# Performance work log

Hardware: AMD Instinct MI355X
Metric: run time of the kernel (lower is better)

Reference implementation:

```python
import jax, jax.numpy as jnp
import numpy as np

N_NODES = 50000
N_EDGES = 800000
F_IN = 128
HEADS = 4
C = 64  # hidden_dim // heads
HIDDEN = HEADS * C
NUM_GRAPHS = 256
NEG_SLOPE = 0.2


def setup_inputs() -> dict:
    key = jax.random.key(0)
    ks = jax.random.split(key, 10)
    x = jax.random.normal(ks[0], (N_NODES, F_IN), dtype=jnp.float32)
    edge_index = jax.random.randint(ks[1], (2, N_EDGES), 0, N_NODES, dtype=jnp.int64)
    edge_attr = jax.random.normal(ks[2], (N_EDGES, 8), dtype=jnp.float32)
    batch = jnp.sort(jax.random.randint(ks[3], (N_NODES,), 0, NUM_GRAPHS, dtype=jnp.int64))
    # GATConv params (PyG: lin weight, att_src/att_dst, bias) + fc head
    W = jax.random.normal(ks[4], (F_IN, HIDDEN), dtype=jnp.float32) / np.sqrt(F_IN)
    att_src = jax.random.normal(ks[5], (HEADS, C), dtype=jnp.float32) / np.sqrt(C)
    att_dst = jax.random.normal(ks[6], (HEADS, C), dtype=jnp.float32) / np.sqrt(C)
    bias = jax.random.normal(ks[7], (HIDDEN,), dtype=jnp.float32) * 0.01
    fc_w = jax.random.normal(ks[8], (1, HIDDEN), dtype=jnp.float32) / np.sqrt(HIDDEN)
    fc_b = jax.random.normal(ks[9], (1,), dtype=jnp.float32) * 0.01
    return {"x": x, "edge_index": edge_index, "edge_attr": edge_attr, "batch": batch,
            "W": W, "att_src": att_src, "att_dst": att_dst, "bias": bias,
            "fc_w": fc_w, "fc_b": fc_b}


def reference(x, edge_index, edge_attr, batch, W, att_src, att_dst, bias, fc_w, fc_b):
    N = x.shape[0]
    # add self loops
    loops = jnp.arange(N, dtype=edge_index.dtype)
    src = jnp.concatenate([edge_index[0], loops])  # [E+N]
    dst = jnp.concatenate([edge_index[1], loops])
    # GATConv: linear transform per head
    h = (x @ W).reshape(N, HEADS, C)  # [N,H,C]
    a_src = jnp.einsum('nhc,hc->nh', h, att_src)  # [N,H]
    a_dst = jnp.einsum('nhc,hc->nh', h, att_dst)
    e = a_src[src] + a_dst[dst]  # [E,H]
    e = jnp.where(e > 0, e, NEG_SLOPE * e)  # leaky_relu
    # segment softmax over destination neighborhoods (self loops guarantee nonempty)
    m = jax.ops.segment_max(e, dst, num_segments=N)
    ee = jnp.exp(e - m[dst])
    s = jax.ops.segment_sum(ee, dst, num_segments=N)
    alpha = ee / s[dst]  # [E,H]
    msg = h[src] * alpha[:, :, None]  # [E,H,C]
    out = jax.ops.segment_sum(msg, dst, num_segments=N).reshape(N, HIDDEN) + bias
    out = jax.nn.elu(out)
    # global mean pool
    sums = jax.ops.segment_sum(out, batch, num_segments=NUM_GRAPHS)
    counts = jax.ops.segment_sum(jnp.ones((N,), out.dtype), batch, num_segments=NUM_GRAPHS)
    pooled = sums / jnp.maximum(counts, 1.0)[:, None]  # [G,HIDDEN]
    o = pooled @ fc_w.T + fc_b  # [G,1]
    return o.reshape(-1)
```

## Files before the change

kernel.cpp:

```cpp
#include <hip/hip_runtime.h>
#include <hip/hip_bf16.h>
#include <math.h>

#define HEADS   4
#define HIDDEN  256
#define FIN     128
#define NGRAPH  256
#define WPB     4
#define HISTB   512
#define PCHUNK  64

using frag_ab = __attribute__((ext_vector_type(8))) short;
using frag_cd = __attribute__((ext_vector_type(4))) float;

__device__ __forceinline__ float bf2f(unsigned short u) {
  union { unsigned int i; float f; } v; v.i = ((unsigned int)u) << 16; return v.f;
}
__device__ __forceinline__ unsigned short f2bf(float f) {
  union { float f; unsigned int i; } v; v.f = f;
  unsigned int b = v.i;
  b += 0x7FFFu + ((b >> 16) & 1u);
  return (unsigned short)(b >> 16);
}

__global__ __launch_bounds__(256) void k_prep(const float* __restrict__ W,
                                              unsigned short* __restrict__ Bf)
{
  int id = blockIdx.x * 256 + threadIdx.x;
  if (id >= 16 * 4 * 64) return;
  int l = id & 63, ks = (id >> 6) & 3, nfg = id >> 8;
  int col = nfg * 16 + (l & 15);
  int k0  = ks * 32 + (l >> 4) * 8;
  unsigned short v[8];
  #pragma unroll
  for (int j = 0; j < 8; ++j) v[j] = f2bf(W[(k0 + j) * HIDDEN + col]);
  *(uint4*)(Bf + (size_t)id * 8) = *(const uint4*)v;
}

__global__ __launch_bounds__(256) void k_gemmhist(
    const float* __restrict__ x, const unsigned short* __restrict__ Bf,
    const float* __restrict__ att_s, const float* __restrict__ att_d,
    unsigned short* __restrict__ h16, float* __restrict__ a_src, float* __restrict__ a_dst,
    const int* __restrict__ ei, int* __restrict__ count,
    int nNodes, int E, int gemmBlocks)
{
  __shared__ unsigned short As[32 * FIN];
  const int t = threadIdx.x;

  if (blockIdx.x >= gemmBlocks) {
    int i = (blockIdx.x - gemmBlocks) * 256 + t;
    int stride = HISTB * 256;
    for (int e = i; e < E; e += stride) atomicAdd(&count[ei[E + e]], 1);
    return;
  }

  const int n0 = blockIdx.x * 32;

  {
    const int row = t >> 3;
    const int g   = n0 + row;
    const int c0  = (t & 7) * 16;
    float4 f0, f1, f2, f3;
    if (g < nNodes) {
      const float* xr = x + (size_t)g * FIN + c0;
      f0 = *(const float4*)(xr + 0);  f1 = *(const float4*)(xr + 4);
      f2 = *(const float4*)(xr + 8);  f3 = *(const float4*)(xr + 12);
    } else {
      f0 = f1 = f2 = f3 = make_float4(0.f, 0.f, 0.f, 0.f);
    }
    unsigned short u[16];
    u[0]=f2bf(f0.x); u[1]=f2bf(f0.y); u[2]=f2bf(f0.z); u[3]=f2bf(f0.w);
    u[4]=f2bf(f1.x); u[5]=f2bf(f1.y); u[6]=f2bf(f1.z); u[7]=f2bf(f1.w);
    u[8]=f2bf(f2.x); u[9]=f2bf(f2.y); u[10]=f2bf(f2.z); u[11]=f2bf(f2.w);
    u[12]=f2bf(f3.x); u[13]=f2bf(f3.y); u[14]=f2bf(f3.z); u[15]=f2bf(f3.w);
    const int sw = (row & 7) << 4;
    char* base = (char*)As + row * 256;
    *(uint4*)(base + (((t & 7) * 32)      ^ sw)) = *(const uint4*)(u + 0);
    *(uint4*)(base + (((t & 7) * 32 + 16) ^ sw)) = *(const uint4*)(u + 8);
  }
  __syncthreads();

  const int w    = t >> 6;
  const int l    = t & 63;
  const int lrow = l & 15;

  frag_ab bfr[4][4];
  #pragma unroll
  for (int nf = 0; nf < 4; ++nf)
    #pragma unroll
    for (int ks = 0; ks < 4; ++ks)
      bfr[nf][ks] = *(const frag_ab*)(Bf + (size_t)(((w * 4 + nf) * 4 + ks) * 64 + l) * 8);

  frag_ab afr[2][4];
  const int lsw = (lrow & 7) << 4;
  #pragma unroll
  for (int mf = 0; mf < 2; ++mf)
    #pragma unroll
    for (int ks = 0; ks < 4; ++ks) {
      int byte = (mf * 16 + lrow) * 256 + ((ks * 64 + (l >> 4) * 16) ^ lsw);
      afr[mf][ks] = *(const frag_ab*)((const char*)As + byte);
    }

  frag_cd acc[2][4];
  #pragma unroll
  for (int mf = 0; mf < 2; ++mf)
    #pragma unroll
    for (int nf = 0; nf < 4; ++nf)
      acc[mf][nf] = (frag_cd){0.f, 0.f, 0.f, 0.f};
  #pragma unroll
  for (int ks = 0; ks < 4; ++ks)
    #pragma unroll
    for (int mf = 0; mf < 2; ++mf)
      #pragma unroll
      for (int nf = 0; nf < 4; ++nf)
        acc[mf][nf] = __builtin_amdgcn_mfma_f32_16x16x32_bf16(
            afr[mf][ks], bfr[nf][ks], acc[mf][nf], 0, 0, 0);

  float asw[4], adw[4];
  #pragma unroll
  for (int nf = 0; nf < 4; ++nf) {
    asw[nf] = att_s[w * 64 + nf * 16 + lrow];
    adw[nf] = att_d[w * 64 + nf * 16 + lrow];
  }

  #pragma unroll
  for (int mf = 0; mf < 2; ++mf) {
    #pragma unroll
    for (int r = 0; r < 4; ++r) {
      const int rowg = n0 + mf * 16 + (l >> 4) * 4 + r;
      if (rowg < nNodes) {
        #pragma unroll
        for (int nf = 0; nf < 4; ++nf)
          h16[(size_t)rowg * HIDDEN + w * 64 + nf * 16 + lrow] = f2bf(acc[mf][nf][r]);
      }
      float ss = 0.f, sd = 0.f;
      #pragma unroll
      for (int nf = 0; nf < 4; ++nf) {
        ss = fmaf(acc[mf][nf][r], asw[nf], ss);
        sd = fmaf(acc[mf][nf][r], adw[nf], sd);
      }
      #pragma unroll
      for (int off2 = 1; off2 <= 8; off2 <<= 1) {
        ss += __shfl_xor(ss, off2, 64);
        sd += __shfl_xor(sd, off2, 64);
      }
      if (lrow == 0 && rowg < nNodes) {
        a_src[rowg * HEADS + w] = ss;
        a_dst[rowg * HEADS + w] = sd;
      }
    }
  }
}

__global__ __launch_bounds__(256) void k_scan1(const int* __restrict__ cnt,
                                               int* __restrict__ offs,
                                               int* __restrict__ bsum, int n)
{
  int t = threadIdx.x, b = blockIdx.x;
  int i = b * 256 + t;
  int v = (i < n) ? cnt[i] + 1 : 0;
  int sc = v;
  #pragma unroll
  for (int d2 = 1; d2 < 64; d2 <<= 1) {
    int u = __shfl_up(sc, d2, 64);
    if ((t & 63) >= d2) sc += u;
  }
  __shared__ int wsum[4];
  if ((t & 63) == 63) wsum[t >> 6] = sc;
  __syncthreads();
  int base = 0;
  for (int w = 0; w < (t >> 6); ++w) base += wsum[w];
  int incl = sc + base;
  if (i < n) offs[i] = incl - v;
  if (t == 255) bsum[b] = incl;
}

__global__ __launch_bounds__(256) void k_scan23(int* __restrict__ offs,
                                                const int* __restrict__ bsum,
                                                int* __restrict__ cursor,
                                                int n, int nb, int total)
{
  int t = threadIdx.x, b = blockIdx.x;
  float dummy; (void)dummy;
  int partial = 0;
  for (int j = t; j < b; j += 256) partial += bsum[j];
  #pragma unroll
  for (int off2 = 32; off2; off2 >>= 1) partial += __shfl_xor(partial, off2, 64);
  __shared__ int ws4[4];
  if ((t & 63) == 0) ws4[t >> 6] = partial;
  __syncthreads();
  int blockBase = ws4[0] + ws4[1] + ws4[2] + ws4[3];

  int i = b * 256 + t;
  if (i < n) {
    int o = offs[i] + blockBase;
    offs[i] = o;
    cursor[i] = o;
  }
  if (i == 0) offs[n] = total;
}

__global__ __launch_bounds__(256) void k_scatter(
    const int* __restrict__ ei, int* __restrict__ cursor,
    int* __restrict__ ssrc, int E, int N)
{
  int e = blockIdx.x * 256 + threadIdx.x;
  int tot = E + N;
  if (e >= tot) return;
  int s, d;
  if (e < E) { s = ei[e]; d = ei[E + e]; }
  else       { s = e - E; d = s; }
  int pos = atomicAdd(&cursor[d], 1);
  ssrc[pos] = s;
}

__global__ __launch_bounds__(256) void k_agg(
    const unsigned short* __restrict__ h16, const int* __restrict__ offs,
    const int* __restrict__ ssrc,
    const float* __restrict__ a_src, const float* __restrict__ a_dst,
    const float* __restrict__ bias,
    unsigned short* __restrict__ outn, int N)
{
  const int wid0 = blockIdx.x * WPB + (threadIdx.x >> 6);
  if (wid0 >= N) return;
  const int wid  = __builtin_amdgcn_readfirstlane(wid0);
  const int lane = threadIdx.x & 63;
  const int head = lane >> 4;
  const int col  = lane << 2;

  const int beg = offs[wid], end = offs[wid + 1];
  const float ad = a_dst[wid * 4 + head];

  float4 acc = make_float4(0.f, 0.f, 0.f, 0.f);
  float den = 0.f;
  int k = beg;

  for (; k + 8 <= end; k += 8) {
    int s0 = ssrc[k + 0], s1 = ssrc[k + 1], s2 = ssrc[k + 2], s3 = ssrc[k + 3];
    int s4 = ssrc[k + 4], s5 = ssrc[k + 5], s6 = ssrc[k + 6], s7 = ssrc[k + 7];
    float e0 = a_src[s0 * 4 + head], e1 = a_src[s1 * 4 + head];
    float e2 = a_src[s2 * 4 + head], e3 = a_src[s3 * 4 + head];
    float e4 = a_src[s4 * 4 + head], e5 = a_src[s5 * 4 + head];
    float e6 = a_src[s6 * 4 + head], e7 = a_src[s7 * 4 + head];
    ushort4 h0 = *(const ushort4*)(h16 + (size_t)s0 * HIDDEN + col);
    ushort4 h1 = *(const ushort4*)(h16 + (size_t)s1 * HIDDEN + col);
    ushort4 h2 = *(const ushort4*)(h16 + (size_t)s2 * HIDDEN + col);
    ushort4 h3 = *(const ushort4*)(h16 + (size_t)s3 * HIDDEN + col);
    ushort4 h4 = *(const ushort4*)(h16 + (size_t)s4 * HIDDEN + col);
    ushort4 h5 = *(const ushort4*)(h16 + (size_t)s5 * HIDDEN + col);
    ushort4 h6 = *(const ushort4*)(h16 + (size_t)s6 * HIDDEN + col);
    ushort4 h7 = *(const ushort4*)(h16 + (size_t)s7 * HIDDEN + col);
    float w0, w1, w2, w3, w4, w5, w6, w7;
    e0 += ad; e0 = e0 > 0.f ? e0 : 0.2f * e0; w0 = __expf(e0);
    e1 += ad; e1 = e1 > 0.f ? e1 : 0.2f * e1; w1 = __expf(e1);
    e2 += ad; e2 = e2 > 0.f ? e2 : 0.2f * e2; w2 = __expf(e2);
    e3 += ad; e3 = e3 > 0.f ? e3 : 0.2f * e3; w3 = __expf(e3);
    e4 += ad; e4 = e4 > 0.f ? e4 : 0.2f * e4; w4 = __expf(e4);
    e5 += ad; e5 = e5 > 0.f ? e5 : 0.2f * e5; w5 = __expf(e5);
    e6 += ad; e6 = e6 > 0.f ? e6 : 0.2f * e6; w6 = __expf(e6);
    e7 += ad; e7 = e7 > 0.f ? e7 : 0.2f * e7; w7 = __expf(e7);
    den += ((w0 + w1) + (w2 + w3)) + ((w4 + w5) + (w6 + w7));
    acc.x = fmaf(bf2f(h0.x), w0, acc.x); acc.y = fmaf(bf2f(h0.y), w0, acc.y);
    acc.z = fmaf(bf2f(h0.z), w0, acc.z); acc.w = fmaf(bf2f(h0.w), w0, acc.w);
    acc.x = fmaf(bf2f(h1.x), w1, acc.x); acc.y = fmaf(bf2f(h1.y), w1, acc.y);
    acc.z = fmaf(bf2f(h1.z), w1, acc.z); acc.w = fmaf(bf2f(h1.w), w1, acc.w);
    acc.x = fmaf(bf2f(h2.x), w2, acc.x); acc.y = fmaf(bf2f(h2.y), w2, acc.y);
    acc.z = fmaf(bf2f(h2.z), w2, acc.z); acc.w = fmaf(bf2f(h2.w), w2, acc.w);
    acc.x = fmaf(bf2f(h3.x), w3, acc.x); acc.y = fmaf(bf2f(h3.y), w3, acc.y);
    acc.z = fmaf(bf2f(h3.z), w3, acc.z); acc.w = fmaf(bf2f(h3.w), w3, acc.w);
    acc.x = fmaf(bf2f(h4.x), w4, acc.x); acc.y = fmaf(bf2f(h4.y), w4, acc.y);
    acc.z = fmaf(bf2f(h4.z), w4, acc.z); acc.w = fmaf(bf2f(h4.w), w4, acc.w);
    acc.x = fmaf(bf2f(h5.x), w5, acc.x); acc.y = fmaf(bf2f(h5.y), w5, acc.y);
    acc.z = fmaf(bf2f(h5.z), w5, acc.z); acc.w = fmaf(bf2f(h5.w), w5, acc.w);
    acc.x = fmaf(bf2f(h6.x), w6, acc.x); acc.y = fmaf(bf2f(h6.y), w6, acc.y);
    acc.z = fmaf(bf2f(h6.z), w6, acc.z); acc.w = fmaf(bf2f(h6.w), w6, acc.w);
    acc.x = fmaf(bf2f(h7.x), w7, acc.x); acc.y = fmaf(bf2f(h7.y), w7, acc.y);
    acc.z = fmaf(bf2f(h7.z), w7, acc.z); acc.w = fmaf(bf2f(h7.w), w7, acc.w);
  }
  for (; k < end; ++k) {
    int s = ssrc[k];
    float e = a_src[s * 4 + head] + ad;
    e = e > 0.f ? e : 0.2f * e;
    float w = __expf(e);
    ushort4 hv = *(const ushort4*)(h16 + (size_t)s * HIDDEN + col);
    den += w;
    acc.x = fmaf(bf2f(hv.x), w, acc.x); acc.y = fmaf(bf2f(hv.y), w, acc.y);
    acc.z = fmaf(bf2f(hv.z), w, acc.z); acc.w = fmaf(bf2f(hv.w), w, acc.w);
  }

  const float inv = 1.f / den;
  float4 bv = *(const float4*)&bias[col];
  float4 o;
  o.x = fmaf(acc.x, inv, bv.x); o.x = o.x > 0.f ? o.x : expm1f(o.x);
  o.y = fmaf(acc.y, inv, bv.y); o.y = o.y > 0.f ? o.y : expm1f(o.y);
  o.z = fmaf(acc.z, inv, bv.z); o.z = o.z > 0.f ? o.z : expm1f(o.z);
  o.w = fmaf(acc.w, inv, bv.w); o.w = o.w > 0.f ? o.w : expm1f(o.w);

  ushort4 ov;
  ov.x = f2bf(o.x); ov.y = f2bf(o.y); ov.z = f2bf(o.z); ov.w = f2bf(o.w);
  *(ushort4*)(outn + (size_t)wid * HIDDEN + col) = ov;
}

__global__ __launch_bounds__(256) void k_poolp(
    const unsigned short* __restrict__ outn, const int* __restrict__ batch,
    float* __restrict__ pooled, float* __restrict__ cntg, int N)
{
  const int t = threadIdx.x;
  const int n0 = blockIdx.x * PCHUNK;
  if (n0 >= N) return;
  const int n1 = (n0 + PCHUNK < N) ? n0 + PCHUNK : N;

  int cur = batch[n0];
  float run = 0.f;
  int runlen = 0;
  int n = n0;
  for (; n + 4 <= n1; n += 4) {
    unsigned short r0 = outn[(size_t)(n + 0) * HIDDEN + t];
    unsigned short r1 = outn[(size_t)(n + 1) * HIDDEN + t];
    unsigned short r2 = outn[(size_t)(n + 2) * HIDDEN + t];
    unsigned short r3 = outn[(size_t)(n + 3) * HIDDEN + t];
    int g0 = batch[n + 0], g3 = batch[n + 3];
    if (g0 == cur && g3 == cur) {
      run += (bf2f(r0) + bf2f(r1)) + (bf2f(r2) + bf2f(r3));
      runlen += 4;
    } else {
      unsigned short rr[4] = {r0, r1, r2, r3};
      #pragma unroll
      for (int j = 0; j < 4; ++j) {
        int g = batch[n + j];
        if (g != cur) {
          atomicAdd(&pooled[cur * HIDDEN + t], run);
          if (t == 0) atomicAdd(&cntg[cur], (float)runlen);
          run = 0.f; runlen = 0; cur = g;
        }
        run += bf2f(rr[j]); runlen++;
      }
    }
  }
  for (; n < n1; ++n) {
    int g = batch[n];
    if (g != cur) {
      atomicAdd(&pooled[cur * HIDDEN + t], run);
      if (t == 0) atomicAdd(&cntg[cur], (float)runlen);
      run = 0.f; runlen = 0; cur = g;
    }
    run += bf2f(outn[(size_t)n * HIDDEN + t]); runlen++;
  }
  atomicAdd(&pooled[cur * HIDDEN + t], run);
  if (t == 0) atomicAdd(&cntg[cur], (float)runlen);
}

__global__ __launch_bounds__(64) void k_fc(
    const float* __restrict__ pooled, const float* __restrict__ cntg,
    const float* __restrict__ fc_w, const float* __restrict__ fc_b, float* __restrict__ out)
{
  int g = blockIdx.x, l = threadIdx.x;
  float acc = 0.f;
  #pragma unroll
  for (int j = 0; j < HIDDEN / 64; ++j) acc += pooled[g * HIDDEN + j * 64 + l] * fc_w[j * 64 + l];
  #pragma unroll
  for (int off2 = 32; off2; off2 >>= 1) acc += __shfl_xor(acc, off2, 64);
  if (l == 0) out[g] = acc / fmaxf(cntg[g], 1.0f) + fc_b[0];
}

extern "C" void kernel_launch(void* const* d_in, const int* in_sizes, int n_in,
                              void* d_out, int out_size, void* d_ws, size_t ws_size,
                              hipStream_t stream)
{
  const float* x     = (const float*)d_in[0];
  const int*   ei    = (const int*)  d_in[1];
  const int*   batch = (const int*)  d_in[3];
  const float* W     = (const float*)d_in[4];
  const float* att_s = (const float*)d_in[5];
  const float* att_d = (const float*)d_in[6];
  const float* bias  = (const float*)d_in[7];
  const float* fc_w  = (const float*)d_in[8];
  const float* fc_b  = (const float*)d_in[9];
  float* out = (float*)d_out;

  const int N   = in_sizes[0] / FIN;
  const int E   = in_sizes[1] / 2;
  const int TOT = E + N;

  char* p = (char*)d_ws;
  size_t o = 0;
  auto alloc = [&](size_t bytes) -> void* {
    void* r = p + o;
    o = (o + bytes + 255) & ~(size_t)255;
    return r;
  };
  int*   count  = (int*)  alloc((size_t)N * sizeof(int));
  float* pooled = (float*)alloc((size_t)NGRAPH * HIDDEN * sizeof(float));
  float* cntg   = (float*)alloc((size_t)NGRAPH * sizeof(float));
  size_t zeroBytes = o;
  unsigned short* h16 = (unsigned short*)alloc((size_t)N * HIDDEN * sizeof(unsigned short));
  unsigned short* Bf  = (unsigned short*)alloc((size_t)FIN * HIDDEN * sizeof(unsigned short));
  float* a_src  = (float*)alloc((size_t)N * 4 * sizeof(float));
  float* a_dst  = (float*)alloc((size_t)N * 4 * sizeof(float));
  int*   offs   = (int*)  alloc((size_t)(N + 1) * sizeof(int));
  int*   cursor = (int*)  alloc((size_t)N * sizeof(int));
  int*   bsum   = (int*)  alloc(4096);
  int*   ssrc   = (int*)  alloc((size_t)TOT * sizeof(int));
  unsigned short* outn = (unsigned short*)alloc((size_t)N * HIDDEN * sizeof(unsigned short));
  (void)n_in; (void)out_size; (void)ws_size;

  (void)hipMemsetAsync(d_ws, 0, zeroBytes, stream);

  const int gemmBlocks = (N + 31) / 32;
  hipLaunchKernelGGL(k_prep, dim3(16), dim3(256), 0, stream, W, Bf);
  hipLaunchKernelGGL(k_gemmhist, dim3(gemmBlocks + HISTB), dim3(256), 0, stream,
                     x, Bf, att_s, att_d, h16, a_src, a_dst, ei, count, N, E, gemmBlocks);
  const int sb = (N + 255) / 256;
  hipLaunchKernelGGL(k_scan1, dim3(sb), dim3(256), 0, stream, count, offs, bsum, N);
  hipLaunchKernelGGL(k_scan23, dim3(sb), dim3(256), 0, stream, offs, bsum, cursor, N, sb, TOT);
  hipLaunchKernelGGL(k_scatter, dim3((TOT + 255) / 256), dim3(256), 0, stream,
                     ei, cursor, ssrc, E, N);
  hipLaunchKernelGGL(k_agg, dim3((N + WPB - 1) / WPB), dim3(256), 0, stream,
                     h16, offs, ssrc, a_src, a_dst, bias, outn, N);
  hipLaunchKernelGGL(k_poolp, dim3((N + PCHUNK - 1) / PCHUNK), dim3(256), 0, stream,
                     outn, batch, pooled, cntg, N);
  hipLaunchKernelGGL(k_fc, dim3(NGRAPH), dim3(64), 0, stream,
                     pooled, cntg, fc_w, fc_b, out);
}
```

Baseline: 276.9 us.

## Precompute edge attention weights in scatter, merge scans, deepen agg gather unroll

Computes the per-edge exp(leaky_relu(a_src+a_dst)) for all four heads in the scatter kernel and stores it as a float4 per CSR slot, so the aggregation kernel reads weights contiguously instead of gathering a_src and recomputing exp per lane. Merges the two scan kernels into one, where each block sums all preceding counts directly, removing a launch at the cost of O(N) redundant reads per block. The aggregation loop is unrolled to 16 with a 4-wide tail to expose more outstanding gathers. It adds a 16-byte-per-edge write and read of the weight array, plus more register pressure from the wider unroll.

```diff
diff --git a/kernel.cpp b/kernel.cpp
--- a/kernel.cpp
+++ b/kernel.cpp
@@ -152,13 +152,23 @@
   }
 }
 
-__global__ __launch_bounds__(256) void k_scan1(const int* __restrict__ cnt,
-                                               int* __restrict__ offs,
-                                               int* __restrict__ bsum, int n)
-{
-  int t = threadIdx.x, b = blockIdx.x;
-  int i = b * 256 + t;
-  int v = (i < n) ? cnt[i] + 1 : 0;
+__global__ __launch_bounds__(256) void k_scan(const int* __restrict__ cnt,
+                                              int* __restrict__ offs,
+                                              int* __restrict__ cursor,
+                                              int n, int total)
+{
+  const int t = threadIdx.x, b = blockIdx.x;
+  int partial = 0;
+  for (int j = t; j < b * 256; j += 256) partial += cnt[j];
+  #pragma unroll
+  for (int off2 = 32; off2; off2 >>= 1) partial += __shfl_xor(partial, off2, 64);
+  __shared__ int bs4[4];
+  if ((t & 63) == 0) bs4[t >> 6] = partial;
+  __syncthreads();
+  const int base = bs4[0] + bs4[1] + bs4[2] + bs4[3] + b * 256;
+
+  const int i = b * 256 + t;
+  const int v = (i < n) ? cnt[i] + 1 : 0;
   int sc = v;
   #pragma unroll
   for (int d2 = 1; d2 < 64; d2 <<= 1) {
@@ -168,41 +178,18 @@
   __shared__ int wsum[4];
   if ((t & 63) == 63) wsum[t >> 6] = sc;
   __syncthreads();
-  int base = 0;
-  for (int w = 0; w < (t >> 6); ++w) base += wsum[w];
-  int incl = sc + base;
-  if (i < n) offs[i] = incl - v;
-  if (t == 255) bsum[b] = incl;
-}
-
-__global__ __launch_bounds__(256) void k_scan23(int* __restrict__ offs,
-                                                const int* __restrict__ bsum,
-                                                int* __restrict__ cursor,
-                                                int n, int nb, int total)
-{
-  int t = threadIdx.x, b = blockIdx.x;
-  float dummy; (void)dummy;
-  int partial = 0;
-  for (int j = t; j < b; j += 256) partial += bsum[j];
-  #pragma unroll
-  for (int off2 = 32; off2; off2 >>= 1) partial += __shfl_xor(partial, off2, 64);
-  __shared__ int ws4[4];
-  if ((t & 63) == 0) ws4[t >> 6] = partial;
-  __syncthreads();
-  int blockBase = ws4[0] + ws4[1] + ws4[2] + ws4[3];
-
-  int i = b * 256 + t;
-  if (i < n) {
-    int o = offs[i] + blockBase;
-    offs[i] = o;
-    cursor[i] = o;
-  }
+  int wb = 0;
+  for (int w = 0; w < (t >> 6); ++w) wb += wsum[w];
+  const int excl = base + wb + sc - v;
+  if (i < n) { offs[i] = excl; cursor[i] = excl; }
   if (i == 0) offs[n] = total;
 }
 
 __global__ __launch_bounds__(256) void k_scatter(
-    const int* __restrict__ ei, int* __restrict__ cursor,
-    int* __restrict__ ssrc, int E, int N)
+    const int* __restrict__ ei,
+    const float4* __restrict__ a_src4, const float4* __restrict__ a_dst4,
+    int* __restrict__ cursor,
+    int* __restrict__ ssrc, float4* __restrict__ see, int E, int N)
 {
   int e = blockIdx.x * 256 + threadIdx.x;
   int tot = E + N;
@@ -210,14 +197,21 @@
   int s, d;
   if (e < E) { s = ei[e]; d = ei[E + e]; }
   else       { s = e - E; d = s; }
+  float4 as = a_src4[s];
+  float4 ad = a_dst4[d];
+  float4 w; float v;
+  v = as.x + ad.x; v = v > 0.f ? v : 0.2f * v; w.x = __expf(v);
+  v = as.y + ad.y; v = v > 0.f ? v : 0.2f * v; w.y = __expf(v);
+  v = as.z + ad.z; v = v > 0.f ? v : 0.2f * v; w.z = __expf(v);
+  v = as.w + ad.w; v = v > 0.f ? v : 0.2f * v; w.w = __expf(v);
   int pos = atomicAdd(&cursor[d], 1);
   ssrc[pos] = s;
+  see[pos] = w;
 }
 
 __global__ __launch_bounds__(256) void k_agg(
     const unsigned short* __restrict__ h16, const int* __restrict__ offs,
-    const int* __restrict__ ssrc,
-    const float* __restrict__ a_src, const float* __restrict__ a_dst,
+    const int* __restrict__ ssrc, const float* __restrict__ see,
     const float* __restrict__ bias,
     unsigned short* __restrict__ outn, int N)
 {
@@ -229,59 +223,54 @@
   const int col  = lane << 2;
 
   const int beg = offs[wid], end = offs[wid + 1];
-  const float ad = a_dst[wid * 4 + head];
 
   float4 acc = make_float4(0.f, 0.f, 0.f, 0.f);
   float den = 0.f;
   int k = beg;
 
-  for (; k + 8 <= end; k += 8) {
-    int s0 = ssrc[k + 0], s1 = ssrc[k + 1], s2 = ssrc[k + 2], s3 = ssrc[k + 3];
-    int s4 = ssrc[k + 4], s5 = ssrc[k + 5], s6 = ssrc[k + 6], s7 = ssrc[k + 7];
-    float e0 = a_src[s0 * 4 + head], e1 = a_src[s1 * 4 + head];
-    float e2 = a_src[s2 * 4 + head], e3 = a_src[s3 * 4 + head];
-    float e4 = a_src[s4 * 4 + head], e5 = a_src[s5 * 4 + head];
-    float e6 = a_src[s6 * 4 + head], e7 = a_src[s7 * 4 + head];
-    ushort4 h0 = *(const ushort4*)(h16 + (size_t)s0 * HIDDEN + col);
-    ushort4 h1 = *(const ushort4*)(h16 + (size_t)s1 * HIDDEN + col);
-    ushort4 h2 = *(const ushort4*)(h16 + (size_t)s2 * HIDDEN + col);
-    ushort4 h3 = *(const ushort4*)(h16 + (size_t)s3 * HIDDEN + col);
-    ushort4 h4 = *(const ushort4*)(h16 + (size_t)s4 * HIDDEN + col);
-    ushort4 h5 = *(const ushort4*)(h16 + (size_t)s5 * HIDDEN + col);
-    ushort4 h6 = *(const ushort4*)(h16 + (size_t)s6 * HIDDEN + col);
-    ushort4 h7 = *(const ushort4*)(h16 + (size_t)s7 * HIDDEN + col);
-    float w0, w1, w2, w3, w4, w5, w6, w7;
-    e0 += ad; e0 = e0 > 0.f ? e0 : 0.2f * e0; w0 = __expf(e0);
-    e1 += ad; e1 = e1 > 0.f ? e1 : 0.2f * e1; w1 = __expf(e1);
-    e2 += ad; e2 = e2 > 0.f ? e2 : 0.2f * e2; w2 = __expf(e2);
-    e3 += ad; e3 = e3 > 0.f ? e3 : 0.2f * e3; w3 = __expf(e3);
-    e4 += ad; e4 = e4 > 0.f ? e4 : 0.2f * e4; w4 = __expf(e4);
-    e5 += ad; e5 = e5 > 0.f ? e5 : 0.2f * e5; w5 = __expf(e5);
-    e6 += ad; e6 = e6 > 0.f ? e6 : 0.2f * e6; w6 = __expf(e6);
-    e7 += ad; e7 = e7 > 0.f ? e7 : 0.2f * e7; w7 = __expf(e7);
-    den += ((w0 + w1) + (w2 + w3)) + ((w4 + w5) + (w6 + w7));
-    acc.x = fmaf(bf2f(h0.x), w0, acc.x); acc.y = fmaf(bf2f(h0.y), w0, acc.y);
-    acc.z = fmaf(bf2f(h0.z), w0, acc.z); acc.w = fmaf(bf2f(h0.w), w0, acc.w);
-    acc.x = fmaf(bf2f(h1.x), w1, acc.x); acc.y = fmaf(bf2f(h1.y), w1, acc.y);
-    acc.z = fmaf(bf2f(h1.z), w1, acc.z); acc.w = fmaf(bf2f(h1.w), w1, acc.w);
-    acc.x = fmaf(bf2f(h2.x), w2, acc.x); acc.y = fmaf(bf2f(h2.y), w2, acc.y);
-    acc.z = fmaf(bf2f(h2.z), w2, acc.z); acc.w = fmaf(bf2f(h2.w), w2, acc.w);
-    acc.x = fmaf(bf2f(h3.x), w3, acc.x); acc.y = fmaf(bf2f(h3.y), w3, acc.y);
-    acc.z = fmaf(bf2f(h3.z), w3, acc.z); acc.w = fmaf(bf2f(h3.w), w3, acc.w);
-    acc.x = fmaf(bf2f(h4.x), w4, acc.x); acc.y = fmaf(bf2f(h4.y), w4, acc.y);
-    acc.z = fmaf(bf2f(h4.z), w4, acc.z); acc.w = fmaf(bf2f(h4.w), w4, acc.w);
-    acc.x = fmaf(bf2f(h5.x), w5, acc.x); acc.y = fmaf(bf2f(h5.y), w5, acc.y);
-    acc.z = fmaf(bf2f(h5.z), w5, acc.z); acc.w = fmaf(bf2f(h5.w), w5, acc.w);
-    acc.x = fmaf(bf2f(h6.x), w6, acc.x); acc.y = fmaf(bf2f(h6.y), w6, acc.y);
-    acc.z = fmaf(bf2f(h6.z), w6, acc.z); acc.w = fmaf(bf2f(h6.w), w6, acc.w);
-    acc.x = fmaf(bf2f(h7.x), w7, acc.x); acc.y = fmaf(bf2f(h7.y), w7, acc.y);
-    acc.z = fmaf(bf2f(h7.z), w7, acc.z); acc.w = fmaf(bf2f(h7.w), w7, acc.w);
+  for (; k + 16 <= end; k += 16) {
+    int s[16];
+    #pragma unroll
+    for (int j = 0; j < 16; ++j) s[j] = ssrc[k + j];
+    float w[16];
+    #pragma unroll
+    for (int j = 0; j < 16; ++j) w[j] = see[(size_t)(k + j) * 4 + head];
+    ushort4 hv[16];
+    #pragma unroll
+    for (int j = 0; j < 16; ++j)
+      hv[j] = *(const ushort4*)(h16 + (size_t)s[j] * HIDDEN + col);
+    #pragma unroll
+    for (int j = 0; j < 16; ++j) {
+      den += w[j];
+      acc.x = fmaf(bf2f(hv[j].x), w[j], acc.x);
+      acc.y = fmaf(bf2f(hv[j].y), w[j], acc.y);
+      acc.z = fmaf(bf2f(hv[j].z), w[j], acc.z);
+      acc.w = fmaf(bf2f(hv[j].w), w[j], acc.w);
+    }
+  }
+  for (; k + 4 <= end; k += 4) {
+    int s[4];
+    #pragma unroll
+    for (int j = 0; j < 4; ++j) s[j] = ssrc[k + j];
+    float w[4];
+    #pragma unroll
+    for (int j = 0; j < 4; ++j) w[j] = see[(size_t)(k + j) * 4 + head];
+    ushort4 hv[4];
+    #pragma unroll
+    for (int j = 0; j < 4; ++j)
+      hv[j] = *(const ushort4*)(h16 + (size_t)s[j] * HIDDEN + col);
+    #pragma unroll
+    for (int j = 0; j < 4; ++j) {
+      den += w[j];
+      acc.x = fmaf(bf2f(hv[j].x), w[j], acc.x);
+      acc.y = fmaf(bf2f(hv[j].y), w[j], acc.y);
+      acc.z = fmaf(bf2f(hv[j].z), w[j], acc.z);
+      acc.w = fmaf(bf2f(hv[j].w), w[j], acc.w);
+    }
   }
   for (; k < end; ++k) {
     int s = ssrc[k];
-    float e = a_src[s * 4 + head] + ad;
-    e = e > 0.f ? e : 0.2f * e;
-    float w = __expf(e);
+    float w = see[(size_t)k * 4 + head];
     ushort4 hv = *(const ushort4*)(h16 + (size_t)s * HIDDEN + col);
     den += w;
     acc.x = fmaf(bf2f(hv.x), w, acc.x); acc.y = fmaf(bf2f(hv.y), w, acc.y);
@@ -399,8 +388,8 @@
   float* a_dst  = (float*)alloc((size_t)N * 4 * sizeof(float));
   int*   offs   = (int*)  alloc((size_t)(N + 1) * sizeof(int));
   int*   cursor = (int*)  alloc((size_t)N * sizeof(int));
-  int*   bsum   = (int*)  alloc(4096);
   int*   ssrc   = (int*)  alloc((size_t)TOT * sizeof(int));
+  float* see    = (float*)alloc((size_t)TOT * 4 * sizeof(float));
   unsigned short* outn = (unsigned short*)alloc((size_t)N * HIDDEN * sizeof(unsigned short));
   (void)n_in; (void)out_size; (void)ws_size;
 
@@ -411,12 +400,12 @@
   hipLaunchKernelGGL(k_gemmhist, dim3(gemmBlocks + HISTB), dim3(256), 0, stream,
                      x, Bf, att_s, att_d, h16, a_src, a_dst, ei, count, N, E, gemmBlocks);
   const int sb = (N + 255) / 256;
-  hipLaunchKernelGGL(k_scan1, dim3(sb), dim3(256), 0, stream, count, offs, bsum, N);
-  hipLaunchKernelGGL(k_scan23, dim3(sb), dim3(256), 0, stream, offs, bsum, cursor, N, sb, TOT);
+  hipLaunchKernelGGL(k_scan, dim3(sb), dim3(256), 0, stream, count, offs, cursor, N, TOT);
   hipLaunchKernelGGL(k_scatter, dim3((TOT + 255) / 256), dim3(256), 0, stream,
-                     ei, cursor, ssrc, E, N);
+                     ei, (const float4*)a_src, (const float4*)a_dst, cursor, ssrc,
+                     (float4*)see, E, N);
   hipLaunchKernelGGL(k_agg, dim3((N + WPB - 1) / WPB), dim3(256), 0, stream,
-                     h16, offs, ssrc, a_src, a_dst, bias, outn, N);
+                     h16, offs, ssrc, see, bias, outn, N);
   hipLaunchKernelGGL(k_poolp, dim3((N + PCHUNK - 1) / PCHUNK), dim3(256), 0, stream,
                      outn, batch, pooled, cntg, N);
   hipLaunchKernelGGL(k_fc, dim3(NGRAPH), dim3(64), 0, stream,
```

New measurement: 295.0 us. 1.07x slower.
